# Kernel optimization log

Measured on AMD Instinct MI355X. Metric: run time of the kernel, lower is better.

## Reference

```python
import jax, jax.numpy as jnp
import numpy as np

EPS = 1e-7  # K.epsilon()
ROUTINGS = 3


def squash(v, axis=-1):
    s2 = jnp.sum(jnp.square(v), axis=axis, keepdims=True)
    scale = s2 / (1.0 + s2) / jnp.sqrt(s2 + EPS)
    return scale * v


def setup_inputs() -> dict:
    key = jax.random.key(0)
    k1, k2 = jax.random.split(key)
    B, I, D, O, K = 64, 2048, 8, 32, 16
    x = jax.random.normal(k1, (B, I, D), dtype=jnp.float32)
    W = jax.random.normal(k2, (I, O, D, K), dtype=jnp.float32) * 0.05
    return {"x": x, "W": W}


def reference(x, W):
    # u_hat[b,o,i,k] = sum_d x[b,i,d] * W[i,o,d,k]
    u_hat = jnp.einsum('bid,iodk->boik', x, W)  # [B, O, I, K]
    B, O, I, _ = u_hat.shape
    b = jnp.zeros((B, O, I), dtype=u_hat.dtype)
    v = None
    for i in range(ROUTINGS):
        c = jax.nn.softmax(b, axis=1)                      # over output capsules
        s = jnp.einsum('boi,boik->bok', c, u_hat)          # weighted sum
        v = squash(s)                                      # [B, O, K]
        if i < ROUTINGS - 1:
            agreement = jnp.einsum('boik,bok->boi', u_hat, v)
            b = b + agreement
    return v
```

## Files before the change

kernel.cpp:

```cpp
#include <hip/hip_runtime.h>


__device__ __forceinline__ float4 f4add(float4 a, float4 b) {
    return make_float4(a.x + b.x, a.y + b.y, a.z + b.z, a.w + b.w);
}

template<int PASS0>
__global__ __launch_bounds__(512, 4)
void pass_kernel(const float* __restrict__ x,
                 const float* __restrict__ W,
                 const float* __restrict__ vin,
                 float* __restrict__ part)
{
    __shared__ __align__(16) float x_lds[32 * 64];
    __shared__ __align__(16) float red[8 * 2 * 512];
    __shared__ __align__(16) float vg[2 * 512];

    const int t  = threadIdx.x;
    const int w  = t >> 6;
    const int l  = t & 63;
    const int o  = l & 31;
    const int kk = l >> 5;
    const int bx = blockIdx.x;
    const int ch = bx & 255;
    const int h  = bx >> 8;
    const int i  = ch * 8 + w;

    float Wr[8][8];
    {
        const float* wp = W + (size_t)(i * 32 + o) * 128 + kk * 8;
        #pragma unroll
        for (int d = 0; d < 8; ++d) {
            float4 a = *(const float4*)(wp + d * 16);
            float4 b = *(const float4*)(wp + d * 16 + 4);
            Wr[d][0] = a.x; Wr[d][1] = a.y; Wr[d][2] = a.z; Wr[d][3] = a.w;
            Wr[d][4] = b.x; Wr[d][5] = b.y; Wr[d][6] = b.z; Wr[d][7] = b.w;
        }
        #pragma unroll
        for (int d = 0; d < 8; ++d)
            #pragma unroll
            for (int j = 0; j < 8; ++j)
                asm volatile("" : "+v"(Wr[d][j]));
    }
    {
        const int f  = t * 4;
        const int bl = f >> 6, r = f & 63;
        *(float4*)&x_lds[f] =
            *(const float4*)(x + (size_t)(h * 32 + bl) * 16384 + ch * 64 + r);
    }

    for (int g = 0; g < 16; ++g) {
        if (!PASS0) {
            if (t < 256) {
                const int bq = t >> 7, idx = t & 127;
                const int b  = h * 32 + g * 2 + bq;
                *(float4*)&vg[bq * 512 + idx * 4] =
                    *(const float4*)(vin + (size_t)b * 512 + idx * 4);
            }
        }
        __syncthreads();

        #pragma unroll
        for (int bq = 0; bq < 2; ++bq) {
            const int bl = g * 2 + bq;
            float4 xa = *(const float4*)&x_lds[bl * 64 + w * 8];
            float4 xb = *(const float4*)&x_lds[bl * 64 + w * 8 + 4];
            float xr[8] = {xa.x, xa.y, xa.z, xa.w, xb.x, xb.y, xb.z, xb.w};
            float uh[8];
            #pragma unroll
            for (int j = 0; j < 8; ++j) uh[j] = 0.f;
            #pragma unroll
            for (int d = 0; d < 8; ++d) {
                #pragma unroll
                for (int j = 0; j < 8; ++j)
                    uh[j] = fmaf(xr[d], Wr[d][j], uh[j]);
            }
            float c;
            if (PASS0) {
                c = 0.03125f;
            } else {
                float logit = 0.f;
                #pragma unroll
                for (int j = 0; j < 8; ++j)
                    logit = fmaf(uh[j], vg[bq * 512 + (kk * 8 + j) * 32 + o], logit);
                logit += __shfl_xor(logit, 32, 64);
                float ex = __expf(logit);
                float sm = ex;
                #pragma unroll
                for (int off = 16; off >= 1; off >>= 1)
                    sm += __shfl_xor(sm, off, 64);
                c = __fdividef(ex, sm);
            }
            #pragma unroll
            for (int j = 0; j < 8; ++j)
                red[(w * 2 + bq) * 512 + (kk * 8 + j) * 32 + o] = c * uh[j];
        }
        __syncthreads();

        if (t < 256) {
            const int bq = t >> 7, e4 = (t & 127) * 4;
            float4 s = make_float4(0.f, 0.f, 0.f, 0.f);
            #pragma unroll
            for (int slot = 0; slot < 8; ++slot)
                s = f4add(s, *(const float4*)&red[(slot * 2 + bq) * 512 + e4]);
            const int b = h * 32 + g * 2 + bq;
            *(float4*)(part + ((size_t)b * 256 + ch) * 512 + e4) = s;
        }
    }
}

template<int PHASE>
__global__ __launch_bounds__(1024)
void reduce_kernel(const float* __restrict__ part,
                   float* __restrict__ vsum,
                   float* __restrict__ out)
{
    __shared__ float sred[512];
    __shared__ float wpart[8][32];
    const int b = blockIdx.x;
    const int t = threadIdx.x;
    const int e = t & 511;
    const int half = t >> 9;

    const float* p0 = part + ((size_t)b * 256 + half * 128) * 512 + e;
    float acc = 0.f;
    #pragma unroll 8
    for (int cc = 0; cc < 128; ++cc)
        acc += p0[(size_t)cc * 512];

    if (half) sred[e] = acc;
    __syncthreads();

    float s = 0.f;
    if (!half) {
        s = acc + sred[e];
        float sq = s * s;
        sq += __shfl_xor(sq, 32, 64);
        if ((t & 63) < 32) wpart[t >> 6][t & 31] = sq;
    }
    __syncthreads();

    if (!half) {
        float n2 = 0.f;
        #pragma unroll
        for (int ww = 0; ww < 8; ++ww) n2 += wpart[ww][t & 31];
        float v = (n2 / (1.f + n2) * rsqrtf(n2 + 1e-7f)) * s;
        if (PHASE == 2)
            out[(size_t)b * 512 + (t & 31) * 16 + (t >> 5)] = v;
        else if (PHASE == 1)
            vsum[(size_t)b * 512 + t] += v;
        else
            vsum[(size_t)b * 512 + t] = v;
    }
}

extern "C" void kernel_launch(void* const* d_in, const int* in_sizes, int n_in,
                              void* d_out, int out_size, void* d_ws, size_t ws_size,
                              hipStream_t stream)
{
    const float* x = (const float*)d_in[0];
    const float* W = (const float*)d_in[1];
    float* out = (float*)d_out;
    char* ws = (char*)d_ws;

    const size_t partB = (size_t)64 * 256 * 512 * 4;
    const size_t vsumB = (size_t)64 * 512 * 4;
    if (ws_size < partB + vsumB) return;

    float* part = (float*)ws;
    float* vsum = (float*)(ws + partB);

    pass_kernel<1><<<512, 512, 0, stream>>>(x, W, vsum, part);
    reduce_kernel<0><<<64, 1024, 0, stream>>>(part, vsum, out);
    pass_kernel<0><<<512, 512, 0, stream>>>(x, W, vsum, part);
    reduce_kernel<1><<<64, 1024, 0, stream>>>(part, vsum, out);
    pass_kernel<0><<<512, 512, 0, stream>>>(x, W, vsum, part);
    reduce_kernel<2><<<64, 1024, 0, stream>>>(part, vsum, out);
}
```

Baseline: 206.2 us.

## Use o-major swizzled LDS layout and spread reduction over more blocks

The per-block shared buffers (vg and red) switch from a k-major stride-32 layout to an o-major layout with an XOR swizzle. Each thread can then read v and write its weighted u_hat as two float4 accesses instead of eight scalar strided ones. The reduce kernel now splits each batch's 512 outputs across 8 blocks of 64 elements, giving 512 blocks instead of 64 so the 16 MB partial-sum read is spread over more CUs. This changes the vsum/out element order to o-major, which matches the reference output layout, and the swizzle adds index arithmetic.

Result: faster. 196.7 us (-4.6%).

```diff
diff --git a/kernel.cpp b/kernel.cpp
--- a/kernel.cpp
+++ b/kernel.cpp
@@ -4,6 +4,7 @@
 __device__ __forceinline__ float4 f4add(float4 a, float4 b) {
     return make_float4(a.x + b.x, a.y + b.y, a.z + b.z, a.w + b.w);
 }
+__device__ __forceinline__ int swz(int f4) { return f4 ^ ((f4 >> 3) & 7); }
 
 template<int PASS0>
 __global__ __launch_bounds__(512, 4)
@@ -25,6 +26,9 @@
     const int ch = bx & 255;
     const int h  = bx >> 8;
     const int i  = ch * 8 + w;
+
+    const int f4a = swz(o * 4 + kk * 2);
+    const int f4b = swz(o * 4 + kk * 2 + 1);
 
     float Wr[8][8];
     {
@@ -54,7 +58,7 @@
             if (t < 256) {
                 const int bq = t >> 7, idx = t & 127;
                 const int b  = h * 32 + g * 2 + bq;
-                *(float4*)&vg[bq * 512 + idx * 4] =
+                *(float4*)&vg[(bq * 128 + swz(idx)) * 4] =
                     *(const float4*)(vin + (size_t)b * 512 + idx * 4);
             }
         }
@@ -79,10 +83,16 @@
             if (PASS0) {
                 c = 0.03125f;
             } else {
-                float logit = 0.f;
-                #pragma unroll
-                for (int j = 0; j < 8; ++j)
-                    logit = fmaf(uh[j], vg[bq * 512 + (kk * 8 + j) * 32 + o], logit);
+                const float4 va = *(const float4*)&vg[(bq * 128 + f4a) * 4];
+                const float4 vb = *(const float4*)&vg[(bq * 128 + f4b) * 4];
+                float logit = uh[0] * va.x;
+                logit = fmaf(uh[1], va.y, logit);
+                logit = fmaf(uh[2], va.z, logit);
+                logit = fmaf(uh[3], va.w, logit);
+                logit = fmaf(uh[4], vb.x, logit);
+                logit = fmaf(uh[5], vb.y, logit);
+                logit = fmaf(uh[6], vb.z, logit);
+                logit = fmaf(uh[7], vb.w, logit);
                 logit += __shfl_xor(logit, 32, 64);
                 float ex = __expf(logit);
                 float sm = ex;
@@ -91,20 +101,23 @@
                     sm += __shfl_xor(sm, off, 64);
                 c = __fdividef(ex, sm);
             }
-            #pragma unroll
-            for (int j = 0; j < 8; ++j)
-                red[(w * 2 + bq) * 512 + (kk * 8 + j) * 32 + o] = c * uh[j];
+            const int rb = (w * 2 + bq) * 128;
+            *(float4*)&red[(rb + f4a) * 4] =
+                make_float4(c * uh[0], c * uh[1], c * uh[2], c * uh[3]);
+            *(float4*)&red[(rb + f4b) * 4] =
+                make_float4(c * uh[4], c * uh[5], c * uh[6], c * uh[7]);
         }
         __syncthreads();
 
         if (t < 256) {
-            const int bq = t >> 7, e4 = (t & 127) * 4;
+            const int bq = t >> 7, j4 = t & 127;
+            const int sj = swz(j4);
             float4 s = make_float4(0.f, 0.f, 0.f, 0.f);
             #pragma unroll
             for (int slot = 0; slot < 8; ++slot)
-                s = f4add(s, *(const float4*)&red[(slot * 2 + bq) * 512 + e4]);
+                s = f4add(s, *(const float4*)&red[((slot * 2 + bq) * 128 + sj) * 4]);
             const int b = h * 32 + g * 2 + bq;
-            *(float4*)(part + ((size_t)b * 256 + ch) * 512 + e4) = s;
+            *(float4*)(part + ((size_t)b * 256 + ch) * 512 + j4 * 4) = s;
         }
     }
 }
@@ -115,42 +128,36 @@
                    float* __restrict__ vsum,
                    float* __restrict__ out)
 {
-    __shared__ float sred[512];
-    __shared__ float wpart[8][32];
-    const int b = blockIdx.x;
-    const int t = threadIdx.x;
-    const int e = t & 511;
-    const int half = t >> 9;
+    __shared__ float sred[16 * 64];
+    const int bx = blockIdx.x;
+    const int b  = bx >> 3;
+    const int q  = bx & 7;
+    const int t  = threadIdx.x;
+    const int e  = t & 63;
+    const int p  = t >> 6;
 
-    const float* p0 = part + ((size_t)b * 256 + half * 128) * 512 + e;
+    const float* p0 = part + ((size_t)b * 256 + p) * 512 + q * 64 + e;
     float acc = 0.f;
-    #pragma unroll 8
-    for (int cc = 0; cc < 128; ++cc)
-        acc += p0[(size_t)cc * 512];
-
-    if (half) sred[e] = acc;
+    #pragma unroll
+    for (int cc = 0; cc < 16; ++cc)
+        acc += p0[(size_t)cc * 16 * 512];
+    sred[p * 64 + e] = acc;
     __syncthreads();
 
-    float s = 0.f;
-    if (!half) {
-        s = acc + sred[e];
+    if (t < 64) {
+        float s = 0.f;
+        #pragma unroll
+        for (int pp = 0; pp < 16; ++pp)
+            s += sred[pp * 64 + t];
         float sq = s * s;
-        sq += __shfl_xor(sq, 32, 64);
-        if ((t & 63) < 32) wpart[t >> 6][t & 31] = sq;
-    }
-    __syncthreads();
-
-    if (!half) {
-        float n2 = 0.f;
         #pragma unroll
-        for (int ww = 0; ww < 8; ++ww) n2 += wpart[ww][t & 31];
-        float v = (n2 / (1.f + n2) * rsqrtf(n2 + 1e-7f)) * s;
-        if (PHASE == 2)
-            out[(size_t)b * 512 + (t & 31) * 16 + (t >> 5)] = v;
-        else if (PHASE == 1)
-            vsum[(size_t)b * 512 + t] += v;
-        else
-            vsum[(size_t)b * 512 + t] = v;
+        for (int off = 8; off >= 1; off >>= 1)
+            sq += __shfl_xor(sq, off, 16);
+        float v = (sq / (1.f + sq) * rsqrtf(sq + 1e-7f)) * s;
+        const size_t idx = (size_t)b * 512 + q * 64 + t;
+        if (PHASE == 2)      out[idx]   = v;
+        else if (PHASE == 1) vsum[idx] += v;
+        else                 vsum[idx]  = v;
     }
 }
 
@@ -171,9 +178,9 @@
     float* vsum = (float*)(ws + partB);
 
     pass_kernel<1><<<512, 512, 0, stream>>>(x, W, vsum, part);
-    reduce_kernel<0><<<64, 1024, 0, stream>>>(part, vsum, out);
+    reduce_kernel<0><<<512, 1024, 0, stream>>>(part, vsum, out);
     pass_kernel<0><<<512, 512, 0, stream>>>(x, W, vsum, part);
-    reduce_kernel<1><<<64, 1024, 0, stream>>>(part, vsum, out);
+    reduce_kernel<1><<<512, 1024, 0, stream>>>(part, vsum, out);
     pass_kernel<0><<<512, 512, 0, stream>>>(x, W, vsum, part);
-    reduce_kernel<2><<<64, 1024, 0, stream>>>(part, vsum, out);
+    reduce_kernel<2><<<512, 1024, 0, stream>>>(part, vsum, out);
 }
```
